# Kernel optimization log

Measured on AMD Instinct MI355X. Metric: run time of the kernel, lower is better.

Reference implementation:

```python
import jax, jax.numpy as jnp
import numpy as np

N = 4096
IN_F = 256
F = 64      # out_features
H = 4       # heads
NEG_SLOPE = 0.2


def setup_inputs() -> dict:
    key = jax.random.key(0)
    k1, k2, k3, k4 = jax.random.split(key, 4)
    x = jax.random.normal(k1, (N, IN_F), dtype=jnp.float32)
    # symmetric random binary adjacency with self-loops (avoids empty softmax rows)
    adj = jax.random.bernoulli(k2, 0.5, (N, N)).astype(jnp.float32)
    adj = jnp.clip(adj + adj.T, 0.0, 1.0)
    adj = jnp.maximum(adj, jnp.eye(N, dtype=jnp.float32))
    W = jax.random.normal(k3, (IN_F, F * H), dtype=jnp.float32) * (1.0 / np.sqrt(IN_F))
    a = jax.random.normal(k4, (2 * F, 1), dtype=jnp.float32) * 0.1
    return {"x": x, "adj": adj, "W": W, "a": a}


def reference(x, adj, W, a):
    # h: [N, H, F]
    h = (x @ W).reshape(N, H, F)
    # e[i, j, h] = leakyrelu(a_l . h[i, h] + a_r . h[j, h])  -- avoids the O(N^2*H*2F) concat
    a_l = a[:F, 0]
    a_r = a[F:, 0]
    el = jnp.einsum('nhf,f->nh', h, a_l)  # [N, H]
    er = jnp.einsum('nhf,f->nh', h, a_r)  # [N, H]
    e = jax.nn.leaky_relu(el[:, None, :] + er[None, :, :], NEG_SLOPE)  # [N, N, H]
    e = jnp.where(adj[:, :, None] == 0, -jnp.inf, e)
    attention = jax.nn.softmax(e, axis=1)  # softmax over neighbors j
    h_prime = jnp.einsum('ijh,jhf->ihf', attention, h)  # [N, H, F]
    return h_prime.mean(axis=1)  # [N, F]  (heads > 1 -> mean over heads)
```

## Files before the change

kernel.cpp:

```cpp
#include <hip/hip_runtime.h>
#include <hip/hip_bf16.h>

#define NN 4096
#define LOG2E 1.44269504088896340736f

typedef __attribute__((ext_vector_type(8))) short s8v;
typedef __attribute__((ext_vector_type(4))) float f4v;

__device__ __forceinline__ unsigned fu(float x){ union{float f;unsigned u;}z; z.f=x; return z.u; }
__device__ __forceinline__ unsigned short f2bf_rne(float x){
  unsigned u = fu(x);
  u += 0x7fffu + ((u >> 16) & 1u);
  return (unsigned short)(u >> 16);
}
__device__ __forceinline__ unsigned pack2_rne(float a, float b){
  return (unsigned)f2bf_rne(a) | ((unsigned)f2bf_rne(b) << 16);
}

__global__ __launch_bounds__(256) void k1_proj(
    const float* __restrict__ x, const float* __restrict__ W,
    const float* __restrict__ a, unsigned short* __restrict__ Vf,
    float* __restrict__ el4, float* __restrict__ Qr, float* __restrict__ Sr)
{
  __shared__ float4 xs[512];
  const int t = threadIdx.x;
  const int r0 = blockIdx.x * 8;
  const float4* xg = (const float4*)(x + (size_t)r0 * 256);
  xs[t] = xg[t];
  xs[t + 256] = xg[t + 256];
  __syncthreads();

  float acc[8] = {0.f,0.f,0.f,0.f,0.f,0.f,0.f,0.f};
  const float* Wp = W + t;
  float wa0 = Wp[0],    wa1 = Wp[256],  wa2 = Wp[512],  wa3 = Wp[768];
  float wb0 = Wp[1024], wb1 = Wp[1280], wb2 = Wp[1536], wb3 = Wp[1792];
  #pragma unroll 1
  for (int k4 = 0; k4 < 64; ++k4) {
    const int kn = (k4 + 2) & 63;
    float nw0 = Wp[kn*1024 +   0];
    float nw1 = Wp[kn*1024 + 256];
    float nw2 = Wp[kn*1024 + 512];
    float nw3 = Wp[kn*1024 + 768];
    #pragma unroll
    for (int r = 0; r < 8; ++r) {
      float4 xv = xs[r*64 + k4];
      acc[r] = fmaf(xv.x, wa0, acc[r]);
      acc[r] = fmaf(xv.y, wa1, acc[r]);
      acc[r] = fmaf(xv.z, wa2, acc[r]);
      acc[r] = fmaf(xv.w, wa3, acc[r]);
    }
    wa0 = wb0; wa1 = wb1; wa2 = wb2; wa3 = wb3;
    wb0 = nw0; wb1 = nw1; wb2 = nw2; wb3 = nw3;
  }

  union { unsigned u[4]; s8v v; } pk;
  #pragma unroll
  for (int p = 0; p < 4; ++p)
    pk.u[p] = pack2_rne(acc[2*p], acc[2*p+1]);
  {
    const int hh = t >> 6, nf = (t >> 4) & 3, mm = t & 15;
    const int jblk = r0 >> 5, qq = (r0 >> 3) & 3;
    const size_t chunk = (size_t)(((hh * 128 + jblk) * 4 + nf) * 64 + qq * 16 + mm);
    *(s8v*)(Vf + chunk * 8) = pk.v;
  }

  const int f = t & 63, h = t >> 6;
  const float al = a[f], ar = a[64 + f];
  #pragma unroll
  for (int r = 0; r < 8; ++r) {
    float v = acc[r] * al;
    float u = acc[r] * ar;
    #pragma unroll
    for (int off = 32; off > 0; off >>= 1) {
      v += __shfl_xor(v, off);
      u += __shfl_xor(u, off);
    }
    if (f == 0) {
      el4[(r0 + r) * 4 + h] = v * LOG2E;
      float up = u * LOG2E;
      Qr[h * NN + (r0 + r)] = __builtin_amdgcn_exp2f(up);
      Sr[h * NN + (r0 + r)] = __builtin_amdgcn_exp2f(0.2f * up);
    }
  }
}

__global__ __launch_bounds__(256, 4) void k0_pack(
    const float* __restrict__ adj, const float* __restrict__ el4,
    const float* __restrict__ Qr, const float* __restrict__ Sr,
    unsigned long long* __restrict__ adjB, float* __restrict__ lsumP)
{
  __shared__ float qsh[8192];
  const int t = threadIdx.x;
  const int w = t >> 6, l = t & 63;
  const int row = blockIdx.x * 4 + w;
  const int p4 = blockIdx.y;
  const int jbase = p4 * 1024;

  const float* arow = adj + (size_t)row * NN + jbase + l * 4;
  float4 av0 = *(const float4*)(arow);
  float4 av1 = *(const float4*)(arow + 256);
  float4 av2 = *(const float4*)(arow + 512);
  float4 av3 = *(const float4*)(arow + 768);

  {
    const int h = t >> 6;
    #pragma unroll
    for (int k = 0; k < 4; ++k) {
      float4 qv = *(const float4*)(Qr + h * NN + jbase + k * 256 + l * 4);
      float4 sv = *(const float4*)(Sr + h * NN + jbase + k * 256 + l * 4);
      *(float4*)(qsh + ((k * 2 + 0) * 4 + h) * 256 + l * 4) = qv;
      *(float4*)(qsh + ((k * 2 + 1) * 4 + h) * 256 + l * 4) = sv;
    }
  }

  {
    unsigned long long* dst = adjB + (size_t)row * 64 + p4 * 16;
    const float4 avs[4] = {av0, av1, av2, av3};
    #pragma unroll
    for (int k = 0; k < 4; ++k) {
      unsigned long long b0 = __ballot(avs[k].x != 0.0f);
      unsigned long long b1 = __ballot(avs[k].y != 0.0f);
      unsigned long long b2 = __ballot(avs[k].z != 0.0f);
      unsigned long long b3 = __ballot(avs[k].w != 0.0f);
      if (l == 0) {
        dst[k * 4 + 0] = b0; dst[k * 4 + 1] = b1;
        dst[k * 4 + 2] = b2; dst[k * 4 + 3] = b3;
      }
    }
  }

  float4 elv = *(const float4*)(el4 + row * 4);
  const float P[4] = { __builtin_amdgcn_exp2f(elv.x), __builtin_amdgcn_exp2f(elv.y),
                       __builtin_amdgcn_exp2f(elv.z), __builtin_amdgcn_exp2f(elv.w) };
  const float R[4] = { __builtin_amdgcn_exp2f(0.2f*elv.x), __builtin_amdgcn_exp2f(0.2f*elv.y),
                       __builtin_amdgcn_exp2f(0.2f*elv.z), __builtin_amdgcn_exp2f(0.2f*elv.w) };

  __syncthreads();

  float ls[4] = {0.f, 0.f, 0.f, 0.f};
  {
    const float4 avs[4] = {av0, av1, av2, av3};
    #pragma unroll
    for (int k = 0; k < 4; ++k) {
      const float4 av = avs[k];
      #pragma unroll
      for (int h = 0; h < 4; ++h) {
        float4 qv = *(const float4*)(qsh + ((k * 2 + 0) * 4 + h) * 256 + l * 4);
        float4 sv = *(const float4*)(qsh + ((k * 2 + 1) * 4 + h) * 256 + l * 4);
        float s;
        s = av.x * fmaxf(P[h] * qv.x, R[h] * sv.x);
        s = fmaf(av.y, fmaxf(P[h] * qv.y, R[h] * sv.y), s);
        s = fmaf(av.z, fmaxf(P[h] * qv.z, R[h] * sv.z), s);
        s = fmaf(av.w, fmaxf(P[h] * qv.w, R[h] * sv.w), s);
        ls[h] += s;
      }
    }
  }
  #pragma unroll
  for (int h = 0; h < 4; ++h) {
    float v = ls[h];
    #pragma unroll
    for (int off = 32; off > 0; off >>= 1) v += __shfl_xor(v, off);
    ls[h] = v;
  }
  if (l == 0)
    *(float4*)(lsumP + ((size_t)p4 * NN + row) * 4) = make_float4(ls[0], ls[1], ls[2], ls[3]);
}

__global__ __launch_bounds__(256, 4) void k2_attn(
    const unsigned long long* __restrict__ adjB, const unsigned short* __restrict__ Vf,
    const float* __restrict__ el4, const float* __restrict__ lsumP,
    const float* __restrict__ Qr, const float* __restrict__ Sr,
    float* __restrict__ out)
{
  __shared__ float qs[8192];
  const int t = threadIdx.x;
  const int w = t >> 6, l = t & 63;
  const int m = l & 15, q = l >> 4;
  const int i0 = blockIdx.x * 16;
  const int sw = blockIdx.y * 4 + w;
  const int i = i0 + m;
  const int jwin = sw * 256;

  {
    const int jc = l >> 3, qq = (l >> 1) & 3, hp = (l & 1) * 4;
    #pragma unroll
    for (int h = 0; h < 4; ++h) {
      float4 qv = *(const float4*)(Qr + h * NN + jwin + l * 4);
      float4 sv = *(const float4*)(Sr + h * NN + jwin + l * 4);
      float* cell = qs + (((w * 4 + h) * 8 + jc) * 4 + qq) * 16;
      *(float4*)(cell + hp) = qv;
      *(float4*)(cell + 8 + hp) = sv;
    }
  }

  float4 elv = *(const float4*)(el4 + i * 4);
  float lx = 0.f, ly = 0.f, lz = 0.f, lw = 0.f;
  #pragma unroll
  for (int p = 0; p < 4; ++p) {
    float4 v = *(const float4*)(lsumP + ((size_t)p * NN + i) * 4);
    lx += v.x; ly += v.y; lz += v.z; lw += v.w;
  }
  float Pl[4], Rl[4];
  {
    const float el_[4] = {elv.x, elv.y, elv.z, elv.w};
    const float lv_[4] = {lx, ly, lz, lw};
    #pragma unroll
    for (int h = 0; h < 4; ++h) {
      const float inv = 1.0f / lv_[h];
      Pl[h] = __builtin_amdgcn_exp2f(el_[h]) * inv;
      Rl[h] = __builtin_amdgcn_exp2f(0.2f * el_[h]) * inv;
    }
  }

  const unsigned long long* bp = adjB + (size_t)i * 64 + sw * 4;
  unsigned long long b0 = bp[0], b1 = bp[1], b2 = bp[2], b3 = bp[3];

  f4v acc[4];
  #pragma unroll
  for (int nf = 0; nf < 4; ++nf) acc[nf] = (f4v){0.f, 0.f, 0.f, 0.f};

  const s8v* vfp = (const s8v*)Vf;
  s8v Bc[4];
  #pragma unroll
  for (int nf = 0; nf < 4; ++nf)
    Bc[nf] = vfp[(size_t)((0 * 128 + sw * 8 + 0) * 4 + nf) * 64 + l];

  #pragma unroll 1
  for (int jc = 0; jc < 8; ++jc) {
    const unsigned sh = jc * 8 + q * 2;
    const unsigned t0 = (unsigned)(b0 >> sh) & 3u;
    const unsigned t1 = (unsigned)(b1 >> sh) & 3u;
    const unsigned t2 = (unsigned)(b2 >> sh) & 3u;
    const unsigned t3 = (unsigned)(b3 >> sh) & 3u;
    float bitf[8];
    bitf[0] = (float)(t0 & 1u); bitf[4] = (float)(t0 >> 1);
    bitf[1] = (float)(t1 & 1u); bitf[5] = (float)(t1 >> 1);
    bitf[2] = (float)(t2 & 1u); bitf[6] = (float)(t2 >> 1);
    bitf[3] = (float)(t3 & 1u); bitf[7] = (float)(t3 >> 1);

    #pragma unroll
    for (int h = 0; h < 4; ++h) {
      const int hn = (h < 3) ? h + 1 : 0;
      const int jcn = (h < 3) ? jc : jc + 1;
      s8v Bn[4];
      #pragma unroll
      for (int nf = 0; nf < 4; ++nf)
        Bn[nf] = vfp[(size_t)((hn * 128 + sw * 8 + jcn) * 4 + nf) * 64 + l];

      const float* cell = qs + (((w * 4 + h) * 8 + jc) * 4 + q) * 16;
      float4 q0  = *(const float4*)(cell);
      float4 q1  = *(const float4*)(cell + 4);
      float4 sv0 = *(const float4*)(cell + 8);
      float4 sv1 = *(const float4*)(cell + 12);
      const float Ph = Pl[h], Rh = Rl[h];
      float s0 = bitf[0] * fmaxf(Ph * q0.x, Rh * sv0.x);
      float s1 = bitf[1] * fmaxf(Ph * q0.y, Rh * sv0.y);
      float s2 = bitf[2] * fmaxf(Ph * q0.z, Rh * sv0.z);
      float s3 = bitf[3] * fmaxf(Ph * q0.w, Rh * sv0.w);
      float s4 = bitf[4] * fmaxf(Ph * q1.x, Rh * sv1.x);
      float s5 = bitf[5] * fmaxf(Ph * q1.y, Rh * sv1.y);
      float s6 = bitf[6] * fmaxf(Ph * q1.z, Rh * sv1.z);
      float s7 = bitf[7] * fmaxf(Ph * q1.w, Rh * sv1.w);
      union { unsigned u[4]; s8v v; } A;
      A.u[0] = pack2_rne(s0, s1);
      A.u[1] = pack2_rne(s2, s3);
      A.u[2] = pack2_rne(s4, s5);
      A.u[3] = pack2_rne(s6, s7);
      #pragma unroll
      for (int nf = 0; nf < 4; ++nf)
        acc[nf] = __builtin_amdgcn_mfma_f32_16x16x32_bf16(A.v, Bc[nf], acc[nf], 0, 0, 0);
      #pragma unroll
      for (int nf = 0; nf < 4; ++nf) Bc[nf] = Bn[nf];
    }
  }

  __syncthreads();
  if (w > 0) {
    float* dst = qs + ((w - 1) * 64 + l) * 20;
    #pragma unroll
    for (int nf = 0; nf < 4; ++nf)
      *(f4v*)(dst + nf * 4) = acc[nf];
  }
  __syncthreads();
  if (w == 0) {
    const float* src = qs + l * 20;
    #pragma unroll
    for (int nf = 0; nf < 4; ++nf) {
      f4v s = acc[nf];
      s += *(const f4v*)(src +    0 + nf * 4);
      s += *(const f4v*)(src + 1280 + nf * 4);
      s += *(const f4v*)(src + 2560 + nf * 4);
      #pragma unroll
      for (int r = 0; r < 4; ++r) {
        int row = i0 + q * 4 + r;
        int col = nf * 16 + m;
        atomicAdd(&out[row * 64 + col], 0.25f * s[r]);
      }
    }
  }
}

extern "C" void kernel_launch(void* const* d_in, const int* in_sizes, int n_in,
                              void* d_out, int out_size, void* d_ws, size_t ws_size,
                              hipStream_t stream) {
  const float* x   = (const float*)d_in[0];
  const float* adj = (const float*)d_in[1];
  const float* W   = (const float*)d_in[2];
  const float* a   = (const float*)d_in[3];
  float* out = (float*)d_out;

  char* ws = (char*)d_ws;
  unsigned short* Vf = (unsigned short*)ws;
  float* el4   = (float*)(ws + (2u << 20));
  float* Qr    = (float*)(ws + (2u << 20) + (64u << 10));
  float* Sr    = (float*)(ws + (2u << 20) + (128u << 10));
  float* lsumP = (float*)(ws + (2u << 20) + (192u << 10));
  unsigned long long* adjB = (unsigned long long*)(ws + (2u << 20) + (448u << 10));

  hipMemsetAsync(out, 0, (size_t)out_size * sizeof(float), stream);
  k1_proj<<<512, 256, 0, stream>>>(x, W, a, Vf, el4, Qr, Sr);
  k0_pack<<<dim3(1024, 4), 256, 0, stream>>>(adj, el4, Qr, Sr, adjB, lsumP);
  k2_attn<<<dim3(256, 4), 256, 0, stream>>>(adjB, Vf, el4, lsumP, Qr, Sr, out);
}
```

Baseline: 159.6 us.

## Process two 16-row tiles per wave in attention kernel to reuse V fragments

```diff
diff --git a/kernel.cpp b/kernel.cpp
--- a/kernel.cpp
+++ b/kernel.cpp
@@ -167,7 +167,7 @@
     *(float4*)(lsumP + ((size_t)p4 * NN + row) * 4) = make_float4(ls[0], ls[1], ls[2], ls[3]);
 }
 
-__global__ __launch_bounds__(256, 4) void k2_attn(
+__global__ __launch_bounds__(256, 2) void k2_attn(
     const unsigned long long* __restrict__ adjB, const unsigned short* __restrict__ Vf,
     const float* __restrict__ el4, const float* __restrict__ lsumP,
     const float* __restrict__ Qr, const float* __restrict__ Sr,
@@ -177,9 +177,8 @@
   const int t = threadIdx.x;
   const int w = t >> 6, l = t & 63;
   const int m = l & 15, q = l >> 4;
-  const int i0 = blockIdx.x * 16;
+  const int i0 = blockIdx.x * 32;
   const int sw = blockIdx.y * 4 + w;
-  const int i = i0 + m;
   const int jwin = sw * 256;
 
   {
@@ -194,31 +193,35 @@
     }
   }
 
-  float4 elv = *(const float4*)(el4 + i * 4);
-  float lx = 0.f, ly = 0.f, lz = 0.f, lw = 0.f;
-  #pragma unroll
-  for (int p = 0; p < 4; ++p) {
-    float4 v = *(const float4*)(lsumP + ((size_t)p * NN + i) * 4);
-    lx += v.x; ly += v.y; lz += v.z; lw += v.w;
-  }
-  float Pl[4], Rl[4];
-  {
+  float Pl[2][4], Rl[2][4];
+  unsigned long long bm[2][4];
+  #pragma unroll
+  for (int s = 0; s < 2; ++s) {
+    const int i = i0 + s * 16 + m;
+    float4 elv = *(const float4*)(el4 + i * 4);
+    float lx = 0.f, ly = 0.f, lz = 0.f, lw = 0.f;
+    #pragma unroll
+    for (int p = 0; p < 4; ++p) {
+      float4 v = *(const float4*)(lsumP + ((size_t)p * NN + i) * 4);
+      lx += v.x; ly += v.y; lz += v.z; lw += v.w;
+    }
     const float el_[4] = {elv.x, elv.y, elv.z, elv.w};
     const float lv_[4] = {lx, ly, lz, lw};
     #pragma unroll
     for (int h = 0; h < 4; ++h) {
       const float inv = 1.0f / lv_[h];
-      Pl[h] = __builtin_amdgcn_exp2f(el_[h]) * inv;
-      Rl[h] = __builtin_amdgcn_exp2f(0.2f * el_[h]) * inv;
-    }
-  }
-
-  const unsigned long long* bp = adjB + (size_t)i * 64 + sw * 4;
-  unsigned long long b0 = bp[0], b1 = bp[1], b2 = bp[2], b3 = bp[3];
-
-  f4v acc[4];
-  #pragma unroll
-  for (int nf = 0; nf < 4; ++nf) acc[nf] = (f4v){0.f, 0.f, 0.f, 0.f};
+      Pl[s][h] = __builtin_amdgcn_exp2f(el_[h]) * inv;
+      Rl[s][h] = __builtin_amdgcn_exp2f(0.2f * el_[h]) * inv;
+    }
+    const unsigned long long* bp = adjB + (size_t)i * 64 + sw * 4;
+    bm[s][0] = bp[0]; bm[s][1] = bp[1]; bm[s][2] = bp[2]; bm[s][3] = bp[3];
+  }
+
+  f4v acc[2][4];
+  #pragma unroll
+  for (int s = 0; s < 2; ++s)
+    #pragma unroll
+    for (int nf = 0; nf < 4; ++nf) acc[s][nf] = (f4v){0.f, 0.f, 0.f, 0.f};
 
   const s8v* vfp = (const s8v*)Vf;
   s8v Bc[4];
@@ -229,15 +232,18 @@
   #pragma unroll 1
   for (int jc = 0; jc < 8; ++jc) {
     const unsigned sh = jc * 8 + q * 2;
-    const unsigned t0 = (unsigned)(b0 >> sh) & 3u;
-    const unsigned t1 = (unsigned)(b1 >> sh) & 3u;
-    const unsigned t2 = (unsigned)(b2 >> sh) & 3u;
-    const unsigned t3 = (unsigned)(b3 >> sh) & 3u;
-    float bitf[8];
-    bitf[0] = (float)(t0 & 1u); bitf[4] = (float)(t0 >> 1);
-    bitf[1] = (float)(t1 & 1u); bitf[5] = (float)(t1 >> 1);
-    bitf[2] = (float)(t2 & 1u); bitf[6] = (float)(t2 >> 1);
-    bitf[3] = (float)(t3 & 1u); bitf[7] = (float)(t3 >> 1);
+    float bitf[2][8];
+    #pragma unroll
+    for (int s = 0; s < 2; ++s) {
+      const unsigned t0 = (unsigned)(bm[s][0] >> sh) & 3u;
+      const unsigned t1 = (unsigned)(bm[s][1] >> sh) & 3u;
+      const unsigned t2 = (unsigned)(bm[s][2] >> sh) & 3u;
+      const unsigned t3 = (unsigned)(bm[s][3] >> sh) & 3u;
+      bitf[s][0] = (float)(t0 & 1u); bitf[s][4] = (float)(t0 >> 1);
+      bitf[s][1] = (float)(t1 & 1u); bitf[s][5] = (float)(t1 >> 1);
+      bitf[s][2] = (float)(t2 & 1u); bitf[s][6] = (float)(t2 >> 1);
+      bitf[s][3] = (float)(t3 & 1u); bitf[s][7] = (float)(t3 >> 1);
+    }
 
     #pragma unroll
     for (int h = 0; h < 4; ++h) {
@@ -253,23 +259,26 @@
       float4 q1  = *(const float4*)(cell + 4);
       float4 sv0 = *(const float4*)(cell + 8);
       float4 sv1 = *(const float4*)(cell + 12);
-      const float Ph = Pl[h], Rh = Rl[h];
-      float s0 = bitf[0] * fmaxf(Ph * q0.x, Rh * sv0.x);
-      float s1 = bitf[1] * fmaxf(Ph * q0.y, Rh * sv0.y);
-      float s2 = bitf[2] * fmaxf(Ph * q0.z, Rh * sv0.z);
-      float s3 = bitf[3] * fmaxf(Ph * q0.w, Rh * sv0.w);
-      float s4 = bitf[4] * fmaxf(Ph * q1.x, Rh * sv1.x);
-      float s5 = bitf[5] * fmaxf(Ph * q1.y, Rh * sv1.y);
-      float s6 = bitf[6] * fmaxf(Ph * q1.z, Rh * sv1.z);
-      float s7 = bitf[7] * fmaxf(Ph * q1.w, Rh * sv1.w);
-      union { unsigned u[4]; s8v v; } A;
-      A.u[0] = pack2_rne(s0, s1);
-      A.u[1] = pack2_rne(s2, s3);
-      A.u[2] = pack2_rne(s4, s5);
-      A.u[3] = pack2_rne(s6, s7);
-      #pragma unroll
-      for (int nf = 0; nf < 4; ++nf)
-        acc[nf] = __builtin_amdgcn_mfma_f32_16x16x32_bf16(A.v, Bc[nf], acc[nf], 0, 0, 0);
+      #pragma unroll
+      for (int s = 0; s < 2; ++s) {
+        const float Ph = Pl[s][h], Rh = Rl[s][h];
+        float s0 = bitf[s][0] * fmaxf(Ph * q0.x, Rh * sv0.x);
+        float s1 = bitf[s][1] * fmaxf(Ph * q0.y, Rh * sv0.y);
+        float s2 = bitf[s][2] * fmaxf(Ph * q0.z, Rh * sv0.z);
+        float s3 = bitf[s][3] * fmaxf(Ph * q0.w, Rh * sv0.w);
+        float s4 = bitf[s][4] * fmaxf(Ph * q1.x, Rh * sv1.x);
+        float s5 = bitf[s][5] * fmaxf(Ph * q1.y, Rh * sv1.y);
+        float s6 = bitf[s][6] * fmaxf(Ph * q1.z, Rh * sv1.z);
+        float s7 = bitf[s][7] * fmaxf(Ph * q1.w, Rh * sv1.w);
+        union { unsigned u[4]; s8v v; } A;
+        A.u[0] = pack2_rne(s0, s1);
+        A.u[1] = pack2_rne(s2, s3);
+        A.u[2] = pack2_rne(s4, s5);
+        A.u[3] = pack2_rne(s6, s7);
+        #pragma unroll
+        for (int nf = 0; nf < 4; ++nf)
+          acc[s][nf] = __builtin_amdgcn_mfma_f32_16x16x32_bf16(A.v, Bc[nf], acc[s][nf], 0, 0, 0);
+      }
       #pragma unroll
       for (int nf = 0; nf < 4; ++nf) Bc[nf] = Bn[nf];
     }
@@ -277,27 +286,30 @@
 
   __syncthreads();
   if (w > 0) {
-    float* dst = qs + ((w - 1) * 64 + l) * 20;
-    #pragma unroll
-    for (int nf = 0; nf < 4; ++nf)
-      *(f4v*)(dst + nf * 4) = acc[nf];
+    float* dst = qs + ((w - 1) * 64 + l) * 36;
+    #pragma unroll
+    for (int s = 0; s < 2; ++s)
+      #pragma unroll
+      for (int nf = 0; nf < 4; ++nf)
+        *(f4v*)(dst + (s * 4 + nf) * 4) = acc[s][nf];
   }
   __syncthreads();
   if (w == 0) {
-    const float* src = qs + l * 20;
-    #pragma unroll
-    for (int nf = 0; nf < 4; ++nf) {
-      f4v s = acc[nf];
-      s += *(const f4v*)(src +    0 + nf * 4);
-      s += *(const f4v*)(src + 1280 + nf * 4);
-      s += *(const f4v*)(src + 2560 + nf * 4);
-      #pragma unroll
-      for (int r = 0; r < 4; ++r) {
-        int row = i0 + q * 4 + r;
-        int col = nf * 16 + m;
-        atomicAdd(&out[row * 64 + col], 0.25f * s[r]);
+    #pragma unroll
+    for (int s = 0; s < 2; ++s)
+      #pragma unroll
+      for (int nf = 0; nf < 4; ++nf) {
+        f4v sum = acc[s][nf];
+        #pragma unroll
+        for (int ww = 0; ww < 3; ++ww)
+          sum += *(const f4v*)(qs + (ww * 64 + l) * 36 + (s * 4 + nf) * 4);
+        #pragma unroll
+        for (int r = 0; r < 4; ++r) {
+          int row = i0 + s * 16 + q * 4 + r;
+          int col = nf * 16 + m;
+          atomicAdd(&out[row * 64 + col], 0.25f * sum[r]);
+        }
       }
-    }
   }
 }
 
@@ -321,5 +333,5 @@
   hipMemsetAsync(out, 0, (size_t)out_size * sizeof(float), stream);
   k1_proj<<<512, 256, 0, stream>>>(x, W, a, Vf, el4, Qr, Sr);
   k0_pack<<<dim3(1024, 4), 256, 0, stream>>>(adj, el4, Qr, Sr, adjB, lsumP);
-  k2_attn<<<dim3(256, 4), 256, 0, stream>>>(adjB, Vf, el4, lsumP, Qr, Sr, out);
-}
+  k2_attn<<<dim3(128, 4), 256, 0, stream>>>(adjB, Vf, el4, lsumP, Qr, Sr, out);
+}
```

Result: no change. 157.5 us (-1.3%).
